# Optimization experiments

Hardware: AMD Instinct MI355X
Metric: run time of the kernel (lower is better)

## Reference

```python
import jax, jax.numpy as jnp
import numpy as np

TOPK = 8
ROUTE_SCALE = 2.5


def setup_inputs() -> dict:
    key = jax.random.key(0)
    k1, k2 = jax.random.split(key)
    N, D, E = 16384, 2048, 64
    x = jax.random.normal(k1, (N, D), dtype=jnp.float32)
    # kaiming_uniform-ish scale for the router weight
    bound = 1.0 / np.sqrt(D)
    weight = jax.random.uniform(k2, (E, D), dtype=jnp.float32, minval=-bound, maxval=bound)
    expert_bias = jnp.zeros((E,), dtype=jnp.float32)
    return {"x": x, "weight": weight, "expert_bias": expert_bias}


def reference(x, weight, expert_bias):
    # linear scorer: (N, D) @ (D, E) -> (N, E)
    scores = jax.nn.sigmoid(jnp.einsum('nd,ed->ne', x.astype(jnp.float32), weight.astype(jnp.float32)))
    original_scores = scores
    # aux-loss-free routing: add dynamic per-expert bias for selection only
    routing_scores = scores + expert_bias[None, :]
    _, indices = jax.lax.top_k(routing_scores, TOPK)          # (N, TOPK) int32
    weights = jnp.take_along_axis(original_scores, indices, axis=1)  # gather original (un-biased) scores
    # sigmoid scoring -> renormalize the selected weights
    weights = weights / (jnp.sum(weights, axis=-1, keepdims=True) + 1e-8)
    weights = weights * ROUTE_SCALE
    return weights.astype(x.dtype), indices
```

## Files before the change

kernel.cpp:

```cpp
#include <hip/hip_runtime.h>
#include <math.h>


#pragma clang fp contract(off)

#define D_DIM 2048
#define E_DIM 64
#define TOPK 8
#define TM 16
#define BK 64
#define NR (D_DIM / BK)
#define XS 68
#define WS 68
#define SCS 65

typedef float v2f __attribute__((ext_vector_type(2)));

__global__ __launch_bounds__(256, 4) void expert_gate_kernel(
    const float* __restrict__ x,
    const float* __restrict__ w,
    const float* __restrict__ bias,
    float* __restrict__ out,
    int N)
{
#pragma clang fp contract(off)
    __shared__ float Xs[TM * XS];
    __shared__ float Ws[E_DIM * WS];
    __shared__ float Sc[TM * SCS];

    const int t    = threadIdx.x;
    const int tx   = t & 15;
    const int ty   = t >> 4;
    const int tok0 = blockIdx.x * TM;
    const int lane = t & 63;
    const float my_bias = bias[lane];

    const int srow = t >> 4;
    const int scol = (t & 15) << 2;
    const float* xp = &x[(size_t)(tok0 + srow) * D_DIM + scol];
    const float* wp = &w[(size_t)srow * D_DIM + scol];
    const int xw = srow * XS + scol;
    const int ww = srow * WS + scol;

    v2f c01[4], c23[4];
    #pragma unroll
    for (int e = 0; e < 4; ++e) { c01[e] = (v2f)(0.f); c23[e] = (v2f)(0.f); }

    for (int s = 0; s < NR; ++s) {
        float4 v = *reinterpret_cast<const float4*>(xp);
        xp += BK;
        *reinterpret_cast<float4*>(&Xs[xw]) = v;
        #pragma unroll
        for (int i = 0; i < 4; ++i) {
            float4 u = *reinterpret_cast<const float4*>(wp + i * 16 * D_DIM);
            *reinterpret_cast<float4*>(&Ws[ww + i * 16 * WS]) = u;
        }
        wp += BK;
        __syncthreads();

        #pragma unroll
        for (int g = 0; g < 4; ++g) {
            float4 xa[4];
            #pragma unroll
            for (int j = 0; j < 4; ++j)
                xa[j] = *reinterpret_cast<const float4*>(
                    &Xs[ty * XS + g * 16 + 4 * j]);
            float4 wb[4][4];
            #pragma unroll
            for (int e = 0; e < 4; ++e)
                #pragma unroll
                for (int j = 0; j < 4; ++j)
                    wb[e][j] = *reinterpret_cast<const float4*>(
                        &Ws[(tx + 16 * e) * WS + g * 16 + 4 * j]);

            #pragma unroll
            for (int j = 3; j >= 0; --j) {
                const v2f xlo = *reinterpret_cast<const v2f*>(&xa[j].x);
                const v2f xhi = *reinterpret_cast<const v2f*>(&xa[j].z);
                #pragma unroll
                for (int e = 0; e < 4; ++e) {
                    const v2f wlo = *reinterpret_cast<const v2f*>(&wb[e][j].x);
                    const v2f whi = *reinterpret_cast<const v2f*>(&wb[e][j].z);
                    c01[e] = c01[e] + xlo * wlo;
                    c23[e] = c23[e] + xhi * whi;
                }
            }
        }
        __syncthreads();
    }

    #pragma unroll
    for (int e = 0; e < 4; ++e) {
        float z = __fadd_rn(__fadd_rn(c01[e].x, c01[e].y),
                            __fadd_rn(c23[e].x, c23[e].y));
        float ez = (float)exp(-(double)z);
        float sg = __fdiv_rn(1.0f, __fadd_rn(1.0f, ez));
        Sc[ty * SCS + (tx + 16 * e)] = sg;
    }
    __syncthreads();

    const int wave = t >> 6;
    for (int r = 0; r < 4; ++r) {
        const int tok = wave * 4 + r;
        const float sg = Sc[tok * SCS + lane];
        float rv = __fadd_rn(sg, my_bias);
        float outw = 0.f;
        int   outi = 0;
        float ssum = 0.f;
        #pragma unroll
        for (int sel = 0; sel < TOPK; ++sel) {
            float vv = rv;
            int   vi = lane;
            #pragma unroll
            for (int off = 1; off < 64; off <<= 1) {
                float ov = __shfl_xor(vv, off);
                int   oi = __shfl_xor(vi, off);
                if (ov > vv || (ov == vv && oi < vi)) { vv = ov; vi = oi; }
            }
            float cs = __shfl(sg, vi);
            ssum = __fadd_rn(ssum, cs);
            if (lane == sel) { outw = cs; outi = vi; }
            if (lane == vi) rv = -INFINITY;
        }
        if (lane < TOPK) {
            const size_t base = (size_t)(tok0 + tok) * TOPK + lane;
            out[base] = __fmul_rn(__fdiv_rn(outw, __fadd_rn(ssum, 1e-8f)), 2.5f);
            out[(size_t)N * TOPK + base] = (float)outi;
        }
    }
}

extern "C" void kernel_launch(void* const* d_in, const int* in_sizes, int n_in,
                              void* d_out, int out_size, void* d_ws, size_t ws_size,
                              hipStream_t stream) {
    const float* x    = (const float*)d_in[0];
    const float* w    = (const float*)d_in[1];
    const float* bias = (const float*)d_in[2];
    float* out = (float*)d_out;
    const int N = in_sizes[0] / D_DIM;
    const int grid = N / TM;
    expert_gate_kernel<<<grid, 256, 0, stream>>>(x, w, bias, out, N);
}
```

Baseline: 318.2 us.

## Stream x directly into registers with double buffering and larger token tiles

Raises the token tile to 32 per block and uses 128 threads. Each thread now holds a 4x4 output tile and reads x straight from global memory into double-buffered registers, so x is no longer staged through shared memory. Weights are staged in 256-wide K chunks, which cuts the number of barriers, and the multiply and add are done with explicit packed-FP32 inline asm. The cost is much higher register pressure at launch_bounds(128,1), fewer threads per block, and uncoalesced per-thread row reads of x.

```diff
diff --git a/kernel.cpp b/kernel.cpp
--- a/kernel.cpp
+++ b/kernel.cpp
@@ -7,16 +7,64 @@
 #define D_DIM 2048
 #define E_DIM 64
 #define TOPK 8
-#define TM 16
-#define BK 64
-#define NR (D_DIM / BK)
-#define XS 68
-#define WS 68
+#define TM 32
+#define MRK 256
+#define NMR (D_DIM / MRK)
+#define NG  (MRK / 16)
+#define WS  260
 #define SCS 65
 
 typedef float v2f __attribute__((ext_vector_type(2)));
 
-__global__ __launch_bounds__(256, 4) void expert_gate_kernel(
+static __device__ __forceinline__ v2f pk_mul(v2f a, v2f b) {
+    v2f d;
+    asm("v_pk_mul_f32 %0, %1, %2" : "=v"(d) : "v"(a), "v"(b));
+    return d;
+}
+static __device__ __forceinline__ v2f pk_add(v2f a, v2f b) {
+    v2f d;
+    asm("v_pk_add_f32 %0, %1, %2" : "=v"(d) : "v"(a), "v"(b));
+    return d;
+}
+
+#define GROUP_COMPUTE(g, XR)                                                   \
+    {                                                                          \
+        float4 wq[4][4];                                                       \
+        _Pragma("unroll")                                                      \
+        for (int e = 0; e < 4; ++e)                                            \
+            _Pragma("unroll")                                                  \
+            for (int j = 0; j < 4; ++j)                                        \
+                wq[e][j] = *reinterpret_cast<const float4*>(                   \
+                    &Wl[(tx + 16 * e) * WS + (g) * 16 + 4 * j]);               \
+        _Pragma("unroll")                                                      \
+        for (int j = 3; j >= 0; --j) {                                         \
+            _Pragma("unroll")                                                  \
+            for (int i = 0; i < 4; ++i) {                                      \
+                const v2f xlo = *reinterpret_cast<const v2f*>(&XR[i][j].x);    \
+                const v2f xhi = *reinterpret_cast<const v2f*>(&XR[i][j].z);    \
+                _Pragma("unroll")                                              \
+                for (int e = 0; e < 4; ++e) {                                  \
+                    const v2f wlo = *reinterpret_cast<const v2f*>(&wq[e][j].x);\
+                    const v2f whi = *reinterpret_cast<const v2f*>(&wq[e][j].z);\
+                    c01[i][e] = pk_add(c01[i][e], pk_mul(xlo, wlo));           \
+                    c23[i][e] = pk_add(c23[i][e], pk_mul(xhi, whi));           \
+                }                                                              \
+            }                                                                  \
+        }                                                                      \
+    }
+
+#define X_LOAD(XR)                                                             \
+    {                                                                          \
+        _Pragma("unroll")                                                      \
+        for (int i = 0; i < 4; ++i) {                                          \
+            _Pragma("unroll")                                                  \
+            for (int j = 0; j < 4; ++j)                                        \
+                XR[i][j] = *reinterpret_cast<const float4*>(xp[i] + 4 * j);    \
+            xp[i] += 16;                                                       \
+        }                                                                      \
+    }
+
+__global__ __launch_bounds__(128, 1) void expert_gate_kernel(
     const float* __restrict__ x,
     const float* __restrict__ w,
     const float* __restrict__ bias,
@@ -24,8 +72,7 @@
     int N)
 {
 #pragma clang fp contract(off)
-    __shared__ float Xs[TM * XS];
-    __shared__ float Ws[E_DIM * WS];
+    __shared__ float Wl[E_DIM * WS];
     __shared__ float Sc[TM * SCS];
 
     const int t    = threadIdx.x;
@@ -35,73 +82,67 @@
     const int lane = t & 63;
     const float my_bias = bias[lane];
 
-    const int srow = t >> 4;
-    const int scol = (t & 15) << 2;
-    const float* xp = &x[(size_t)(tok0 + srow) * D_DIM + scol];
-    const float* wp = &w[(size_t)srow * D_DIM + scol];
-    const int xw = srow * XS + scol;
-    const int ww = srow * WS + scol;
+    const float* xp[4];
+    #pragma unroll
+    for (int i = 0; i < 4; ++i)
+        xp[i] = &x[(size_t)(tok0 + ty + 8 * i) * D_DIM];
 
-    v2f c01[4], c23[4];
+    const int h = t >> 6;
+    const float* wsg = &w[(size_t)h * D_DIM + 4 * lane];
+    float*       wsl = &Wl[h * WS + 4 * lane];
+
+    v2f c01[4][4], c23[4][4];
     #pragma unroll
-    for (int e = 0; e < 4; ++e) { c01[e] = (v2f)(0.f); c23[e] = (v2f)(0.f); }
+    for (int i = 0; i < 4; ++i)
+        #pragma unroll
+        for (int e = 0; e < 4; ++e) { c01[i][e] = (v2f)(0.f); c23[i][e] = (v2f)(0.f); }
 
-    for (int s = 0; s < NR; ++s) {
-        float4 v = *reinterpret_cast<const float4*>(xp);
-        xp += BK;
-        *reinterpret_cast<float4*>(&Xs[xw]) = v;
-        #pragma unroll
-        for (int i = 0; i < 4; ++i) {
-            float4 u = *reinterpret_cast<const float4*>(wp + i * 16 * D_DIM);
-            *reinterpret_cast<float4*>(&Ws[ww + i * 16 * WS]) = u;
-        }
-        wp += BK;
+    float4 XA[4][4], XB[4][4];
+    X_LOAD(XA);
+
+    for (int m = 0; m < NMR; ++m) {
         __syncthreads();
-
-        #pragma unroll
-        for (int g = 0; g < 4; ++g) {
-            float4 xa[4];
+        {
+            const float* gsrc = wsg + (size_t)m * MRK;
             #pragma unroll
-            for (int j = 0; j < 4; ++j)
-                xa[j] = *reinterpret_cast<const float4*>(
-                    &Xs[ty * XS + g * 16 + 4 * j]);
-            float4 wb[4][4];
-            #pragma unroll
-            for (int e = 0; e < 4; ++e)
+            for (int b = 0; b < 4; ++b) {
+                float4 tmp[8];
                 #pragma unroll
-                for (int j = 0; j < 4; ++j)
-                    wb[e][j] = *reinterpret_cast<const float4*>(
-                        &Ws[(tx + 16 * e) * WS + g * 16 + 4 * j]);
-
-            #pragma unroll
-            for (int j = 3; j >= 0; --j) {
-                const v2f xlo = *reinterpret_cast<const v2f*>(&xa[j].x);
-                const v2f xhi = *reinterpret_cast<const v2f*>(&xa[j].z);
+                for (int u = 0; u < 8; ++u)
+                    tmp[u] = *reinterpret_cast<const float4*>(
+                        gsrc + (size_t)(b * 16 + 2 * u) * D_DIM);
                 #pragma unroll
-                for (int e = 0; e < 4; ++e) {
-                    const v2f wlo = *reinterpret_cast<const v2f*>(&wb[e][j].x);
-                    const v2f whi = *reinterpret_cast<const v2f*>(&wb[e][j].z);
-                    c01[e] = c01[e] + xlo * wlo;
-                    c23[e] = c23[e] + xhi * whi;
-                }
+                for (int u = 0; u < 8; ++u)
+                    *reinterpret_cast<float4*>(&wsl[(b * 16 + 2 * u) * WS]) = tmp[u];
             }
         }
         __syncthreads();
+
+        for (int gp = 0; gp < NG / 2; ++gp) {
+            const int g0 = 2 * gp, g1 = 2 * gp + 1;
+            X_LOAD(XB);
+            GROUP_COMPUTE(g0, XA);
+            if (!(m == NMR - 1 && gp == NG / 2 - 1)) { X_LOAD(XA); }
+            GROUP_COMPUTE(g1, XB);
+        }
     }
 
     #pragma unroll
-    for (int e = 0; e < 4; ++e) {
-        float z = __fadd_rn(__fadd_rn(c01[e].x, c01[e].y),
-                            __fadd_rn(c23[e].x, c23[e].y));
-        float ez = (float)exp(-(double)z);
-        float sg = __fdiv_rn(1.0f, __fadd_rn(1.0f, ez));
-        Sc[ty * SCS + (tx + 16 * e)] = sg;
+    for (int i = 0; i < 4; ++i) {
+        #pragma unroll
+        for (int e = 0; e < 4; ++e) {
+            float z = __fadd_rn(__fadd_rn(c01[i][e].x, c01[i][e].y),
+                                __fadd_rn(c23[i][e].x, c23[i][e].y));
+            float ez = (float)exp(-(double)z);
+            float sg = __fdiv_rn(1.0f, __fadd_rn(1.0f, ez));
+            Sc[(ty + 8 * i) * SCS + (tx + 16 * e)] = sg;
+        }
     }
     __syncthreads();
 
     const int wave = t >> 6;
-    for (int r = 0; r < 4; ++r) {
-        const int tok = wave * 4 + r;
+    for (int r = 0; r < 16; ++r) {
+        const int tok = wave * 16 + r;
         const float sg = Sc[tok * SCS + lane];
         float rv = __fadd_rn(sg, my_bias);
         float outw = 0.f;
@@ -139,5 +180,5 @@
     float* out = (float*)d_out;
     const int N = in_sizes[0] / D_DIM;
     const int grid = N / TM;
-    expert_gate_kernel<<<grid, 256, 0, stream>>>(x, w, bias, out, N);
+    expert_gate_kernel<<<grid, 128, 0, stream>>>(x, w, bias, out, N);
 }
```

Result: slower. 442.6 us (+39.1%).
